# Performance work log

Hardware: AMD Instinct MI355X
Metric: run time of the kernel (lower is better)

Reference implementation:

```python
import jax, jax.numpy as jnp
import numpy as np

EPS = 1e-10


def spmm(rows, cols, vals, x, n_rows):
    # COO sparse [n_rows, *] @ dense x : out[r] = sum_e vals[e] * x[cols[e]]
    return jax.ops.segment_sum(vals[:, None] * x[cols], rows, num_segments=n_rows)


def setup_inputs() -> dict:
    key = jax.random.key(0)
    ks = jax.random.split(key, 16)
    n_in, n_full, n_nodes, d, nnz, n_out = 65536, 65536, 131072, 256, 262144, 16384
    return {
        "mu": jax.random.normal(ks[0], (n_in, d), jnp.float32),
        "var": jax.random.uniform(ks[1], (n_in, d), jnp.float32),
        "mu_history": jax.random.normal(ks[2], (n_nodes, d), jnp.float32),
        "var_history": jax.random.uniform(ks[3], (n_nodes, d), jnp.float32),
        "adj_vals": jax.random.uniform(ks[4], (nnz,), jnp.float32),
        "fadj_vals": jax.random.uniform(ks[5], (nnz,), jnp.float32),
        "madj_vals": jax.random.uniform(ks[6], (nnz,), jnp.float32),
        "adj_rows": jax.random.randint(ks[7], (nnz,), 0, n_out, jnp.int32),
        "adj_cols": jax.random.randint(ks[8], (nnz,), 0, n_in, jnp.int32),
        "fadj_rows": jax.random.randint(ks[9], (nnz,), 0, n_out, jnp.int32),
        "fadj_cols": jax.random.randint(ks[10], (nnz,), 0, n_full, jnp.int32),
        "madj_rows": jax.random.randint(ks[11], (nnz,), 0, n_out, jnp.int32),
        "madj_cols": jax.random.randint(ks[12], (nnz,), 0, n_in, jnp.int32),
        "ifield": jax.random.randint(ks[13], (n_in,), 0, n_nodes, jnp.int32),
        "ffield": jax.random.randint(ks[14], (n_full,), 0, n_nodes, jnp.int32),
        "n_out": n_out,
    }


def reference(mu, var, mu_history, var_history,
              adj_vals, fadj_vals, madj_vals,
              adj_rows, adj_cols, fadj_rows, fadj_cols, madj_rows, madj_cols,
              ifield, ffield, n_out):
    # VRAggregator._call, tuple-(mu, var) branch, normalization != 'gcn'
    mu_self = mu[:n_out]
    var_self = var[:n_out]
    delta_mu = mu - mu_history[ifield]          # [n_in, d]
    mu_bar = mu_history[ffield]                 # [n_full, d]
    sigma = jnp.sqrt(var)
    sigma_bar = jnp.sqrt(var_history[ifield])
    delta_sigma = sigma - sigma_bar
    var_bar = var_history[ffield]
    msigma = delta_sigma * sigma_bar
    mu_neighbour = (spmm(adj_rows, adj_cols, adj_vals, delta_mu, n_out)
                    + spmm(fadj_rows, fadj_cols, fadj_vals, mu_bar, n_out))
    var_neighbour = (spmm(adj_rows, adj_cols, adj_vals * adj_vals, delta_sigma * delta_sigma, n_out)
                     + spmm(fadj_rows, fadj_cols, fadj_vals * fadj_vals, var_bar, n_out)
                     + 2.0 * spmm(madj_rows, madj_cols, madj_vals, msigma, n_out))
    var_neighbour = jax.nn.relu(var_neighbour) + EPS
    return (jnp.concatenate((mu_self, mu_neighbour), axis=1),
            jnp.concatenate((var_self, var_neighbour), axis=1))
```

## Files before the change

### kernel.cpp

```cpp
#include <hip/hip_runtime.h>

#define EPS_F 1e-10f

typedef unsigned int u32;

__device__ __forceinline__ u32 bf16pair(float lo, float hi) {
  u32 a = __float_as_uint(lo);
  u32 b = __float_as_uint(hi);
  a = a + 0x7FFFu + ((a >> 16) & 1u);
  b = b + 0x7FFFu + ((b >> 16) & 1u);
  return (a >> 16) | (b & 0xFFFF0000u);
}
__device__ __forceinline__ float bf_lo(u32 u) { return __uint_as_float(u << 16); }
__device__ __forceinline__ float bf_hi(u32 u) { return __uint_as_float(u & 0xFFFF0000u); }

__device__ __forceinline__ void acc_am(float4& am, uint4 u, float W) {
  am.x += W * bf_lo(u.x); am.y += W * bf_hi(u.x);
  am.z += W * bf_lo(u.y); am.w += W * bf_hi(u.y);
}
__device__ __forceinline__ void acc_av(float4& av, uint4 u, float Q) {
  av.x += Q * bf_lo(u.z); av.y += Q * bf_hi(u.z);
  av.z += Q * bf_lo(u.w); av.w += Q * bf_hi(u.w);
}
__device__ __forceinline__ void acc_m(float4& av, uint2 x, float W) {
  av.x += W * bf_lo(x.x); av.y += W * bf_hi(x.x);
  av.z += W * bf_lo(x.y); av.w += W * bf_hi(x.y);
}

__global__ __launch_bounds__(256) void k_count(
    const int* __restrict__ ra, const int* __restrict__ rf,
    const int* __restrict__ rm, int* __restrict__ cnt, int nnz, int n_out) {
  int total = 3 * nnz;
  for (int i = blockIdx.x * blockDim.x + threadIdx.x; i < total;
       i += gridDim.x * blockDim.x) {
    int m = (i >= nnz) + (i >= 2 * nnz);
    int e = i - m * nnz;
    const int* rp = (m == 0) ? ra : (m == 1) ? rf : rm;
    atomicAdd(&cnt[m * n_out + rp[e]], 1);
  }
}

__global__ __launch_bounds__(256) void k_scan3(const int* __restrict__ cnt_all,
                                               int* __restrict__ base_all,
                                               int* __restrict__ cur_all, int n) {
  const int* cnt = cnt_all + blockIdx.x * n;
  int* base = base_all + blockIdx.x * (n + 1);
  int* cur = cur_all + blockIdx.x * n;
  __shared__ int sums[256];
  int tid = threadIdx.x;
  int chunk = (n + 255) / 256;
  int s = tid * chunk, e = min(s + chunk, n);
  int local = 0;
  for (int i = s; i < e; ++i) local += cnt[i];
  sums[tid] = local;
  __syncthreads();
  for (int off = 1; off < 256; off <<= 1) {
    int v = (tid >= off) ? sums[tid - off] : 0;
    __syncthreads();
    sums[tid] += v;
    __syncthreads();
  }
  int run = (tid == 0) ? 0 : sums[tid - 1];
  for (int i = s; i < e; ++i) {
    base[i] = run;
    cur[i] = run;
    run += cnt[i];
  }
  if (tid == 255) base[n] = sums[255];
}

template <bool WITH_FB>
__global__ __launch_bounds__(256) void k_pre_scatter(
    const float* __restrict__ mu, const float* __restrict__ var,
    const float* __restrict__ muh, const float* __restrict__ varh,
    const int* __restrict__ ifield, const int* __restrict__ ffield,
    const int* __restrict__ ra, const int* __restrict__ ca, const float* __restrict__ va,
    const int* __restrict__ rf, const int* __restrict__ cf, const float* __restrict__ vf,
    const int* __restrict__ rm, const int* __restrict__ cm, const float* __restrict__ vm,
    int* __restrict__ cur_all, uint2* __restrict__ ord,
    u32* __restrict__ A, u32* __restrict__ M, u32* __restrict__ FB,
    int n_in, int n_full, int n_out, int nnz) {
  int tid = blockIdx.x * blockDim.x + threadIdx.x;
  int nth = gridDim.x * blockDim.x;

  int total = 3 * nnz;
  for (int i = tid; i < total; i += nth) {
    int m = (i >= nnz) + (i >= 2 * nnz);
    int e = i - m * nnz;
    const int* rp = (m == 0) ? ra : (m == 1) ? rf : rm;
    const int* cp = (m == 0) ? ca : (m == 1) ? cf : cm;
    const float* vp = (m == 0) ? va : (m == 1) ? vf : vm;
    int r = rp[e];
    int c = cp[e];
    float w = vp[e];
    if (!WITH_FB && m == 1) c = ffield[c];
    if (m == 2) w = 2.0f * w;
    int pos = atomicAdd(&cur_all[m * n_out + r], 1);
    ord[(size_t)m * nnz + pos] = make_uint2((u32)c, __float_as_uint(w));
  }

  int wave = tid >> 6;
  int lane = tid & 63;
  int nw = nth >> 6;
  int nr = WITH_FB ? (n_in > n_full ? n_in : n_full) : n_in;
  int rpw = (nr + nw - 1) / nw;
  int r0 = wave * rpw;
  int r1 = min(nr, r0 + rpw);
  for (int row = r0; row < r1; ++row) {
    if (row < n_in) {
      int f = ifield[row];
      float4 m  = ((const float4*)(mu   + (size_t)row * 256))[lane];
      float4 v  = ((const float4*)(var  + (size_t)row * 256))[lane];
      float4 mh = ((const float4*)(muh  + (size_t)f   * 256))[lane];
      float4 vh = ((const float4*)(varh + (size_t)f   * 256))[lane];
      float4 d, q, p;
      float s, sb, ds;
      s = sqrtf(v.x); sb = sqrtf(vh.x); ds = s - sb; d.x = m.x - mh.x; q.x = ds * ds; p.x = ds * sb;
      s = sqrtf(v.y); sb = sqrtf(vh.y); ds = s - sb; d.y = m.y - mh.y; q.y = ds * ds; p.y = ds * sb;
      s = sqrtf(v.z); sb = sqrtf(vh.z); ds = s - sb; d.z = m.z - mh.z; q.z = ds * ds; p.z = ds * sb;
      s = sqrtf(v.w); sb = sqrtf(vh.w); ds = s - sb; d.w = m.w - mh.w; q.w = ds * ds; p.w = ds * sb;
      uint4 au;
      au.x = bf16pair(d.x, d.y);
      au.y = bf16pair(d.z, d.w);
      au.z = bf16pair(q.x, q.y);
      au.w = bf16pair(q.z, q.w);
      ((uint4*)(A + (size_t)row * 256))[lane] = au;
      uint2 mu2;
      mu2.x = bf16pair(p.x, p.y);
      mu2.y = bf16pair(p.z, p.w);
      ((uint2*)(M + (size_t)row * 128))[lane] = mu2;
    }
    if (WITH_FB && row < n_full) {
      int f = ffield[row];
      float4 mb = ((const float4*)(muh  + (size_t)f * 256))[lane];
      float4 vb = ((const float4*)(varh + (size_t)f * 256))[lane];
      uint4 fu;
      fu.x = bf16pair(mb.x, mb.y);
      fu.y = bf16pair(mb.z, mb.w);
      fu.z = bf16pair(vb.x, vb.y);
      fu.w = bf16pair(vb.z, vb.w);
      ((uint4*)(FB + (size_t)row * 256))[lane] = fu;
    }
  }
}

template <bool HAS_FB>
__global__ __launch_bounds__(256) void k_agg(
    const float* __restrict__ mu, const float* __restrict__ var,
    const float* __restrict__ muh, const float* __restrict__ varh,
    const u32* __restrict__ A, const u32* __restrict__ M,
    const u32* __restrict__ FB,
    const int* __restrict__ base_all, const uint2* __restrict__ ord,
    float* __restrict__ out0, float* __restrict__ out1, int n_out, int nnz) {
  int r = (int)((blockIdx.x * blockDim.x + threadIdx.x) >> 6);
  int lane = threadIdx.x & 63;
  if (r >= n_out) return;

  float4 msf = ((const float4*)(mu  + (size_t)r * 256))[lane];
  float4 vsf = ((const float4*)(var + (size_t)r * 256))[lane];

  float4 am = make_float4(0.f, 0.f, 0.f, 0.f);
  float4 av = make_float4(0.f, 0.f, 0.f, 0.f);

  {
    const int* base = base_all;
    const uint2* o = ord;
    int b0 = base[r], b1 = base[r + 1];
    int p = b0;
    for (; p + 3 < b1; p += 4) {
      uint2 cv0 = o[p], cv1 = o[p + 1], cv2 = o[p + 2], cv3 = o[p + 3];
      uint4 u0 = ((const uint4*)(A + (size_t)cv0.x * 256))[lane];
      uint4 u1 = ((const uint4*)(A + (size_t)cv1.x * 256))[lane];
      uint4 u2 = ((const uint4*)(A + (size_t)cv2.x * 256))[lane];
      uint4 u3 = ((const uint4*)(A + (size_t)cv3.x * 256))[lane];
      float w0 = __uint_as_float(cv0.y), w1 = __uint_as_float(cv1.y);
      float w2 = __uint_as_float(cv2.y), w3 = __uint_as_float(cv3.y);
      acc_am(am, u0, w0); acc_am(am, u1, w1); acc_am(am, u2, w2); acc_am(am, u3, w3);
      acc_av(av, u0, w0 * w0); acc_av(av, u1, w1 * w1);
      acc_av(av, u2, w2 * w2); acc_av(av, u3, w3 * w3);
    }
    for (; p < b1; ++p) {
      uint2 cv0 = o[p];
      float w0 = __uint_as_float(cv0.y);
      uint4 u0 = ((const uint4*)(A + (size_t)cv0.x * 256))[lane];
      acc_am(am, u0, w0); acc_av(av, u0, w0 * w0);
    }
  }

  {
    const int* base = base_all + (n_out + 1);
    const uint2* o = ord + (size_t)nnz;
    int b0 = base[r], b1 = base[r + 1];
    int p = b0;
    if (HAS_FB) {
      for (; p + 3 < b1; p += 4) {
        uint2 cv0 = o[p], cv1 = o[p + 1], cv2 = o[p + 2], cv3 = o[p + 3];
        uint4 u0 = ((const uint4*)(FB + (size_t)cv0.x * 256))[lane];
        uint4 u1 = ((const uint4*)(FB + (size_t)cv1.x * 256))[lane];
        uint4 u2 = ((const uint4*)(FB + (size_t)cv2.x * 256))[lane];
        uint4 u3 = ((const uint4*)(FB + (size_t)cv3.x * 256))[lane];
        float w0 = __uint_as_float(cv0.y), w1 = __uint_as_float(cv1.y);
        float w2 = __uint_as_float(cv2.y), w3 = __uint_as_float(cv3.y);
        acc_am(am, u0, w0); acc_am(am, u1, w1); acc_am(am, u2, w2); acc_am(am, u3, w3);
        acc_av(av, u0, w0 * w0); acc_av(av, u1, w1 * w1);
        acc_av(av, u2, w2 * w2); acc_av(av, u3, w3 * w3);
      }
      for (; p < b1; ++p) {
        uint2 cv0 = o[p];
        float w0 = __uint_as_float(cv0.y);
        uint4 u0 = ((const uint4*)(FB + (size_t)cv0.x * 256))[lane];
        acc_am(am, u0, w0); acc_av(av, u0, w0 * w0);
      }
    } else {
      for (; p + 1 < b1; p += 2) {
        uint2 cv0 = o[p], cv1 = o[p + 1];
        float w0 = __uint_as_float(cv0.y), w1 = __uint_as_float(cv1.y);
        float4 m0 = ((const float4*)(muh  + (size_t)cv0.x * 256))[lane];
        float4 v0 = ((const float4*)(varh + (size_t)cv0.x * 256))[lane];
        float4 m1 = ((const float4*)(muh  + (size_t)cv1.x * 256))[lane];
        float4 v1 = ((const float4*)(varh + (size_t)cv1.x * 256))[lane];
        float q0 = w0 * w0, q1 = w1 * w1;
        am.x += w0 * m0.x + w1 * m1.x; am.y += w0 * m0.y + w1 * m1.y;
        am.z += w0 * m0.z + w1 * m1.z; am.w += w0 * m0.w + w1 * m1.w;
        av.x += q0 * v0.x + q1 * v1.x; av.y += q0 * v0.y + q1 * v1.y;
        av.z += q0 * v0.z + q1 * v1.z; av.w += q0 * v0.w + q1 * v1.w;
      }
      if (p < b1) {
        uint2 cv0 = o[p];
        float w0 = __uint_as_float(cv0.y);
        float4 m0 = ((const float4*)(muh  + (size_t)cv0.x * 256))[lane];
        float4 v0 = ((const float4*)(varh + (size_t)cv0.x * 256))[lane];
        float q0 = w0 * w0;
        am.x += w0 * m0.x; am.y += w0 * m0.y; am.z += w0 * m0.z; am.w += w0 * m0.w;
        av.x += q0 * v0.x; av.y += q0 * v0.y; av.z += q0 * v0.z; av.w += q0 * v0.w;
      }
    }
  }

  {
    const int* base = base_all + 2 * (n_out + 1);
    const uint2* o = ord + 2 * (size_t)nnz;
    int b0 = base[r], b1 = base[r + 1];
    int p = b0;
    for (; p + 3 < b1; p += 4) {
      uint2 cv0 = o[p], cv1 = o[p + 1], cv2 = o[p + 2], cv3 = o[p + 3];
      uint2 x0 = ((const uint2*)(M + (size_t)cv0.x * 128))[lane];
      uint2 x1 = ((const uint2*)(M + (size_t)cv1.x * 128))[lane];
      uint2 x2 = ((const uint2*)(M + (size_t)cv2.x * 128))[lane];
      uint2 x3 = ((const uint2*)(M + (size_t)cv3.x * 128))[lane];
      float w0 = __uint_as_float(cv0.y), w1 = __uint_as_float(cv1.y);
      float w2 = __uint_as_float(cv2.y), w3 = __uint_as_float(cv3.y);
      acc_m(av, x0, w0); acc_m(av, x1, w1); acc_m(av, x2, w2); acc_m(av, x3, w3);
    }
    for (; p < b1; ++p) {
      uint2 cv0 = o[p];
      float w0 = __uint_as_float(cv0.y);
      uint2 x0 = ((const uint2*)(M + (size_t)cv0.x * 128))[lane];
      acc_m(av, x0, w0);
    }
  }

  av.x = fmaxf(av.x, 0.f) + EPS_F;
  av.y = fmaxf(av.y, 0.f) + EPS_F;
  av.z = fmaxf(av.z, 0.f) + EPS_F;
  av.w = fmaxf(av.w, 0.f) + EPS_F;
  ((float4*)(out0 + (size_t)r * 512))[lane]       = msf;
  ((float4*)(out0 + (size_t)r * 512 + 256))[lane] = am;
  ((float4*)(out1 + (size_t)r * 512))[lane]       = vsf;
  ((float4*)(out1 + (size_t)r * 512 + 256))[lane] = av;
}

__global__ __launch_bounds__(256) void k_init_out(
    const float* __restrict__ mu, const float* __restrict__ var,
    float* __restrict__ out0, float* __restrict__ out1) {
  int r = blockIdx.x;
  int t = threadIdx.x;
  const float4 z = make_float4(0.f, 0.f, 0.f, 0.f);
  if (t < 128) {
    float4* dst = (float4*)(out0 + (size_t)r * 512);
    dst[t] = (t < 64) ? ((const float4*)(mu + (size_t)r * 256))[t] : z;
  } else {
    int u = t - 128;
    float4* dst = (float4*)(out1 + (size_t)r * 512);
    dst[u] = (u < 64) ? ((const float4*)(var + (size_t)r * 256))[u] : z;
  }
}

__global__ __launch_bounds__(256) void k_edge_adj_fb(
    const float* __restrict__ vals, const int* __restrict__ rows,
    const int* __restrict__ cols,
    const float* __restrict__ mu, const float* __restrict__ var,
    const float* __restrict__ muh, const float* __restrict__ varh,
    const int* __restrict__ ifield,
    float* __restrict__ out0, float* __restrict__ out1, int nnz) {
  int wave = (int)((blockIdx.x * blockDim.x + threadIdx.x) >> 6);
  int lane = threadIdx.x & 63;
  int nw = (int)((gridDim.x * blockDim.x) >> 6);
  for (int e = wave; e < nnz; e += nw) {
    float w = vals[e];
    int r = rows[e];
    int c = cols[e];
    int f = ifield[c];
    float4 m  = ((const float4*)(mu   + (size_t)c * 256))[lane];
    float4 v  = ((const float4*)(var  + (size_t)c * 256))[lane];
    float4 mh = ((const float4*)(muh  + (size_t)f * 256))[lane];
    float4 vh = ((const float4*)(varh + (size_t)f * 256))[lane];
    float4 xm, xv;
    float ds;
    xm.x = m.x - mh.x; ds = sqrtf(v.x) - sqrtf(vh.x); xv.x = ds * ds;
    xm.y = m.y - mh.y; ds = sqrtf(v.y) - sqrtf(vh.y); xv.y = ds * ds;
    xm.z = m.z - mh.z; ds = sqrtf(v.z) - sqrtf(vh.z); xv.z = ds * ds;
    xm.w = m.w - mh.w; ds = sqrtf(v.w) - sqrtf(vh.w); xv.w = ds * ds;
    float w2 = w * w;
    float* om = out0 + (size_t)r * 512 + 256 + lane * 4;
    float* ov = out1 + (size_t)r * 512 + 256 + lane * 4;
    atomicAdd(om + 0, w * xm.x); atomicAdd(om + 1, w * xm.y);
    atomicAdd(om + 2, w * xm.z); atomicAdd(om + 3, w * xm.w);
    atomicAdd(ov + 0, w2 * xv.x); atomicAdd(ov + 1, w2 * xv.y);
    atomicAdd(ov + 2, w2 * xv.z); atomicAdd(ov + 3, w2 * xv.w);
  }
}

__global__ __launch_bounds__(256) void k_edge_fadj_fb(
    const float* __restrict__ vals, const int* __restrict__ rows,
    const int* __restrict__ cols,
    const float* __restrict__ muh, const float* __restrict__ varh,
    const int* __restrict__ ffield,
    float* __restrict__ out0, float* __restrict__ out1, int nnz) {
  int wave = (int)((blockIdx.x * blockDim.x + threadIdx.x) >> 6);
  int lane = threadIdx.x & 63;
  int nw = (int)((gridDim.x * blockDim.x) >> 6);
  for (int e = wave; e < nnz; e += nw) {
    float w = vals[e];
    int r = rows[e];
    int f = ffield[cols[e]];
    float4 mb = ((const float4*)(muh  + (size_t)f * 256))[lane];
    float4 vb = ((const float4*)(varh + (size_t)f * 256))[lane];
    float w2 = w * w;
    float* om = out0 + (size_t)r * 512 + 256 + lane * 4;
    float* ov = out1 + (size_t)r * 512 + 256 + lane * 4;
    atomicAdd(om + 0, w * mb.x); atomicAdd(om + 1, w * mb.y);
    atomicAdd(om + 2, w * mb.z); atomicAdd(om + 3, w * mb.w);
    atomicAdd(ov + 0, w2 * vb.x); atomicAdd(ov + 1, w2 * vb.y);
    atomicAdd(ov + 2, w2 * vb.z); atomicAdd(ov + 3, w2 * vb.w);
  }
}

__global__ __launch_bounds__(256) void k_edge_madj_fb(
    const float* __restrict__ vals, const int* __restrict__ rows,
    const int* __restrict__ cols,
    const float* __restrict__ var, const float* __restrict__ varh,
    const int* __restrict__ ifield,
    float* __restrict__ out1, int nnz) {
  int wave = (int)((blockIdx.x * blockDim.x + threadIdx.x) >> 6);
  int lane = threadIdx.x & 63;
  int nw = (int)((gridDim.x * blockDim.x) >> 6);
  for (int e = wave; e < nnz; e += nw) {
    float w = 2.0f * vals[e];
    int r = rows[e];
    int c = cols[e];
    int f = ifield[c];
    float4 v  = ((const float4*)(var  + (size_t)c * 256))[lane];
    float4 vh = ((const float4*)(varh + (size_t)f * 256))[lane];
    float4 x;
    float sb;
    sb = sqrtf(vh.x); x.x = (sqrtf(v.x) - sb) * sb;
    sb = sqrtf(vh.y); x.y = (sqrtf(v.y) - sb) * sb;
    sb = sqrtf(vh.z); x.z = (sqrtf(v.z) - sb) * sb;
    sb = sqrtf(vh.w); x.w = (sqrtf(v.w) - sb) * sb;
    float* ov = out1 + (size_t)r * 512 + 256 + lane * 4;
    atomicAdd(ov + 0, w * x.x); atomicAdd(ov + 1, w * x.y);
    atomicAdd(ov + 2, w * x.z); atomicAdd(ov + 3, w * x.w);
  }
}

__global__ __launch_bounds__(256) void k_final(float* __restrict__ out1, int n_out) {
  int total = n_out * 64;
  for (int i = blockIdx.x * blockDim.x + threadIdx.x; i < total;
       i += gridDim.x * blockDim.x) {
    int r = i >> 6;
    int q = i & 63;
    float4* p = (float4*)(out1 + (size_t)r * 512 + 256) + q;
    float4 v = *p;
    v.x = fmaxf(v.x, 0.f) + EPS_F;
    v.y = fmaxf(v.y, 0.f) + EPS_F;
    v.z = fmaxf(v.z, 0.f) + EPS_F;
    v.w = fmaxf(v.w, 0.f) + EPS_F;
    *p = v;
  }
}

extern "C" void kernel_launch(void* const* d_in, const int* in_sizes, int n_in_args,
                              void* d_out, int out_size, void* d_ws, size_t ws_size,
                              hipStream_t stream) {
  const float* mu        = (const float*)d_in[0];
  const float* var       = (const float*)d_in[1];
  const float* muh       = (const float*)d_in[2];
  const float* varh      = (const float*)d_in[3];
  const float* adj_vals  = (const float*)d_in[4];
  const float* fadj_vals = (const float*)d_in[5];
  const float* madj_vals = (const float*)d_in[6];
  const int* adj_rows    = (const int*)d_in[7];
  const int* adj_cols    = (const int*)d_in[8];
  const int* fadj_rows   = (const int*)d_in[9];
  const int* fadj_cols   = (const int*)d_in[10];
  const int* madj_rows   = (const int*)d_in[11];
  const int* madj_cols   = (const int*)d_in[12];
  const int* ifield      = (const int*)d_in[13];
  const int* ffield      = (const int*)d_in[14];

  const int n_out  = out_size / 1024;
  const int n_in   = in_sizes[0] / 256;
  const int nnz    = in_sizes[4];
  const int n_full = in_sizes[14];

  float* out0 = (float*)d_out;
  float* out1 = out0 + (size_t)n_out * 512;

  const size_t uA = (size_t)n_in * 256;
  const size_t uM = (size_t)n_in * 128;
  const size_t uFB = (size_t)n_full * 256;
  const size_t uOrd = (size_t)3 * nnz * 2;
  const size_t uCnt = (size_t)3 * n_out;
  const size_t uBase = (size_t)3 * (n_out + 1);
  const size_t need2 = (uA + uM + uOrd + uCnt + uBase + uCnt) * sizeof(u32);
  const size_t need1 = need2 + uFB * sizeof(u32);

  if (ws_size >= need2) {
    const bool fb = (ws_size >= need1);
    u32* A = (u32*)d_ws;
    u32* M = A + uA;
    u32* FB = M + uM;
    u32* tail = fb ? (FB + uFB) : (M + uM);
    uint2* ord = (uint2*)tail;
    int* cnt  = (int*)(tail + uOrd);
    int* base = cnt + uCnt;
    int* cur  = base + uBase;

    (void)hipMemsetAsync(cnt, 0, uCnt * sizeof(int), stream);
    k_count<<<1024, 256, 0, stream>>>(adj_rows, fadj_rows, madj_rows, cnt, nnz, n_out);
    k_scan3<<<3, 256, 0, stream>>>(cnt, base, cur, n_out);
    if (fb) {
      k_pre_scatter<true><<<2048, 256, 0, stream>>>(
          mu, var, muh, varh, ifield, ffield,
          adj_rows, adj_cols, adj_vals, fadj_rows, fadj_cols, fadj_vals,
          madj_rows, madj_cols, madj_vals,
          cur, ord, A, M, FB, n_in, n_full, n_out, nnz);
    } else {
      k_pre_scatter<false><<<2048, 256, 0, stream>>>(
          mu, var, muh, varh, ifield, ffield,
          adj_rows, adj_cols, adj_vals, fadj_rows, fadj_cols, fadj_vals,
          madj_rows, madj_cols, madj_vals,
          cur, ord, A, M, nullptr, n_in, n_full, n_out, nnz);
    }
    int blocks = (n_out * 64 + 255) / 256;
    if (fb) {
      k_agg<true><<<blocks, 256, 0, stream>>>(mu, var, muh, varh, A, M, FB, base, ord,
                                              out0, out1, n_out, nnz);
    } else {
      k_agg<false><<<blocks, 256, 0, stream>>>(mu, var, muh, varh, A, M, nullptr, base, ord,
                                               out0, out1, n_out, nnz);
    }
  } else {
    k_init_out<<<n_out, 256, 0, stream>>>(mu, var, out0, out1);
    k_edge_adj_fb<<<4096, 256, 0, stream>>>(adj_vals, adj_rows, adj_cols,
                                            mu, var, muh, varh, ifield, out0, out1, nnz);
    k_edge_madj_fb<<<4096, 256, 0, stream>>>(madj_vals, madj_rows, madj_cols,
                                             var, varh, ifield, out1, nnz);
    k_edge_fadj_fb<<<4096, 256, 0, stream>>>(fadj_vals, fadj_rows, fadj_cols,
                                             muh, varh, ffield, out0, out1, nnz);
    k_final<<<4096, 256, 0, stream>>>(out1, n_out);
  }
}
```

Measured before the change: 310.7 us.

## Pack full history table to bf16 once and gather through it

Instead of building a per-full-row bf16 FB table (gathering history rows via ffield), the count kernel now converts the entire mu/var history table (n_nodes rows) to packed bf16 in a contiguous streaming pass. The pre-scatter kernel resolves fadj columns through ffield into node indices, and reads the history for delta computation from the bf16 table. This removes a random gather of fp32 history in pre-scatter, but the table now has n_nodes rows instead of n_full, so more bytes are written. Reading history in bf16 before the subtraction and sqrt also adds precision error to delta_mu and sigma_bar.

```diff
diff --git a/kernel.cpp b/kernel.cpp
--- a/kernel.cpp
+++ b/kernel.cpp
@@ -27,16 +27,38 @@
   av.z += W * bf_lo(x.y); av.w += W * bf_hi(x.y);
 }
 
-__global__ __launch_bounds__(256) void k_count(
+template <bool WITH_HB>
+__global__ __launch_bounds__(256) void k_hist_count(
+    const float* __restrict__ muh, const float* __restrict__ varh,
+    u32* __restrict__ HB, int n_nodes,
     const int* __restrict__ ra, const int* __restrict__ rf,
     const int* __restrict__ rm, int* __restrict__ cnt, int nnz, int n_out) {
+  int tid = blockIdx.x * blockDim.x + threadIdx.x;
+  int nth = gridDim.x * blockDim.x;
+
   int total = 3 * nnz;
-  for (int i = blockIdx.x * blockDim.x + threadIdx.x; i < total;
-       i += gridDim.x * blockDim.x) {
+  for (int i = tid; i < total; i += nth) {
     int m = (i >= nnz) + (i >= 2 * nnz);
     int e = i - m * nnz;
     const int* rp = (m == 0) ? ra : (m == 1) ? rf : rm;
     atomicAdd(&cnt[m * n_out + rp[e]], 1);
+  }
+
+  if (WITH_HB) {
+    int wave = tid >> 6, lane = tid & 63, nw = nth >> 6;
+    int rpw = (n_nodes + nw - 1) / nw;
+    int r0 = wave * rpw;
+    int r1 = min(n_nodes, r0 + rpw);
+    for (int node = r0; node < r1; ++node) {
+      float4 mh = ((const float4*)(muh  + (size_t)node * 256))[lane];
+      float4 vh = ((const float4*)(varh + (size_t)node * 256))[lane];
+      uint4 hu;
+      hu.x = bf16pair(mh.x, mh.y);
+      hu.y = bf16pair(mh.z, mh.w);
+      hu.z = bf16pair(vh.x, vh.y);
+      hu.w = bf16pair(vh.z, vh.w);
+      ((uint4*)(HB + (size_t)node * 256))[lane] = hu;
+    }
   }
 }
 
@@ -69,17 +91,18 @@
   if (tid == 255) base[n] = sums[255];
 }
 
-template <bool WITH_FB>
+template <bool WITH_HB>
 __global__ __launch_bounds__(256) void k_pre_scatter(
     const float* __restrict__ mu, const float* __restrict__ var,
     const float* __restrict__ muh, const float* __restrict__ varh,
+    const u32* __restrict__ HB,
     const int* __restrict__ ifield, const int* __restrict__ ffield,
     const int* __restrict__ ra, const int* __restrict__ ca, const float* __restrict__ va,
     const int* __restrict__ rf, const int* __restrict__ cf, const float* __restrict__ vf,
     const int* __restrict__ rm, const int* __restrict__ cm, const float* __restrict__ vm,
     int* __restrict__ cur_all, uint2* __restrict__ ord,
-    u32* __restrict__ A, u32* __restrict__ M, u32* __restrict__ FB,
-    int n_in, int n_full, int n_out, int nnz) {
+    u32* __restrict__ A, u32* __restrict__ M,
+    int n_in, int n_out, int nnz) {
   int tid = blockIdx.x * blockDim.x + threadIdx.x;
   int nth = gridDim.x * blockDim.x;
 
@@ -93,63 +116,54 @@
     int r = rp[e];
     int c = cp[e];
     float w = vp[e];
-    if (!WITH_FB && m == 1) c = ffield[c];
+    if (m == 1) c = ffield[c];
     if (m == 2) w = 2.0f * w;
     int pos = atomicAdd(&cur_all[m * n_out + r], 1);
     ord[(size_t)m * nnz + pos] = make_uint2((u32)c, __float_as_uint(w));
   }
 
-  int wave = tid >> 6;
-  int lane = tid & 63;
-  int nw = nth >> 6;
-  int nr = WITH_FB ? (n_in > n_full ? n_in : n_full) : n_in;
-  int rpw = (nr + nw - 1) / nw;
+  int wave = tid >> 6, lane = tid & 63, nw = nth >> 6;
+  int rpw = (n_in + nw - 1) / nw;
   int r0 = wave * rpw;
-  int r1 = min(nr, r0 + rpw);
+  int r1 = min(n_in, r0 + rpw);
   for (int row = r0; row < r1; ++row) {
-    if (row < n_in) {
-      int f = ifield[row];
-      float4 m  = ((const float4*)(mu   + (size_t)row * 256))[lane];
-      float4 v  = ((const float4*)(var  + (size_t)row * 256))[lane];
-      float4 mh = ((const float4*)(muh  + (size_t)f   * 256))[lane];
-      float4 vh = ((const float4*)(varh + (size_t)f   * 256))[lane];
-      float4 d, q, p;
-      float s, sb, ds;
-      s = sqrtf(v.x); sb = sqrtf(vh.x); ds = s - sb; d.x = m.x - mh.x; q.x = ds * ds; p.x = ds * sb;
-      s = sqrtf(v.y); sb = sqrtf(vh.y); ds = s - sb; d.y = m.y - mh.y; q.y = ds * ds; p.y = ds * sb;
-      s = sqrtf(v.z); sb = sqrtf(vh.z); ds = s - sb; d.z = m.z - mh.z; q.z = ds * ds; p.z = ds * sb;
-      s = sqrtf(v.w); sb = sqrtf(vh.w); ds = s - sb; d.w = m.w - mh.w; q.w = ds * ds; p.w = ds * sb;
-      uint4 au;
-      au.x = bf16pair(d.x, d.y);
-      au.y = bf16pair(d.z, d.w);
-      au.z = bf16pair(q.x, q.y);
-      au.w = bf16pair(q.z, q.w);
-      ((uint4*)(A + (size_t)row * 256))[lane] = au;
-      uint2 mu2;
-      mu2.x = bf16pair(p.x, p.y);
-      mu2.y = bf16pair(p.z, p.w);
-      ((uint2*)(M + (size_t)row * 128))[lane] = mu2;
-    }
-    if (WITH_FB && row < n_full) {
-      int f = ffield[row];
-      float4 mb = ((const float4*)(muh  + (size_t)f * 256))[lane];
-      float4 vb = ((const float4*)(varh + (size_t)f * 256))[lane];
-      uint4 fu;
-      fu.x = bf16pair(mb.x, mb.y);
-      fu.y = bf16pair(mb.z, mb.w);
-      fu.z = bf16pair(vb.x, vb.y);
-      fu.w = bf16pair(vb.z, vb.w);
-      ((uint4*)(FB + (size_t)row * 256))[lane] = fu;
-    }
-  }
-}
-
-template <bool HAS_FB>
+    int f = ifield[row];
+    float4 m  = ((const float4*)(mu  + (size_t)row * 256))[lane];
+    float4 v  = ((const float4*)(var + (size_t)row * 256))[lane];
+    float4 mh, vh;
+    if (WITH_HB) {
+      uint4 h = ((const uint4*)(HB + (size_t)f * 256))[lane];
+      mh = make_float4(bf_lo(h.x), bf_hi(h.x), bf_lo(h.y), bf_hi(h.y));
+      vh = make_float4(bf_lo(h.z), bf_hi(h.z), bf_lo(h.w), bf_hi(h.w));
+    } else {
+      mh = ((const float4*)(muh  + (size_t)f * 256))[lane];
+      vh = ((const float4*)(varh + (size_t)f * 256))[lane];
+    }
+    float4 d, q, p;
+    float s, sb, ds;
+    s = sqrtf(v.x); sb = sqrtf(vh.x); ds = s - sb; d.x = m.x - mh.x; q.x = ds * ds; p.x = ds * sb;
+    s = sqrtf(v.y); sb = sqrtf(vh.y); ds = s - sb; d.y = m.y - mh.y; q.y = ds * ds; p.y = ds * sb;
+    s = sqrtf(v.z); sb = sqrtf(vh.z); ds = s - sb; d.z = m.z - mh.z; q.z = ds * ds; p.z = ds * sb;
+    s = sqrtf(v.w); sb = sqrtf(vh.w); ds = s - sb; d.w = m.w - mh.w; q.w = ds * ds; p.w = ds * sb;
+    uint4 au;
+    au.x = bf16pair(d.x, d.y);
+    au.y = bf16pair(d.z, d.w);
+    au.z = bf16pair(q.x, q.y);
+    au.w = bf16pair(q.z, q.w);
+    ((uint4*)(A + (size_t)row * 256))[lane] = au;
+    uint2 mu2;
+    mu2.x = bf16pair(p.x, p.y);
+    mu2.y = bf16pair(p.z, p.w);
+    ((uint2*)(M + (size_t)row * 128))[lane] = mu2;
+  }
+}
+
+template <bool HAS_HB>
 __global__ __launch_bounds__(256) void k_agg(
     const float* __restrict__ mu, const float* __restrict__ var,
     const float* __restrict__ muh, const float* __restrict__ varh,
     const u32* __restrict__ A, const u32* __restrict__ M,
-    const u32* __restrict__ FB,
+    const u32* __restrict__ HB,
     const int* __restrict__ base_all, const uint2* __restrict__ ord,
     float* __restrict__ out0, float* __restrict__ out1, int n_out, int nnz) {
   int r = (int)((blockIdx.x * blockDim.x + threadIdx.x) >> 6);
@@ -192,13 +206,13 @@
     const uint2* o = ord + (size_t)nnz;
     int b0 = base[r], b1 = base[r + 1];
     int p = b0;
-    if (HAS_FB) {
+    if (HAS_HB) {
       for (; p + 3 < b1; p += 4) {
         uint2 cv0 = o[p], cv1 = o[p + 1], cv2 = o[p + 2], cv3 = o[p + 3];
-        uint4 u0 = ((const uint4*)(FB + (size_t)cv0.x * 256))[lane];
-        uint4 u1 = ((const uint4*)(FB + (size_t)cv1.x * 256))[lane];
-        uint4 u2 = ((const uint4*)(FB + (size_t)cv2.x * 256))[lane];
-        uint4 u3 = ((const uint4*)(FB + (size_t)cv3.x * 256))[lane];
+        uint4 u0 = ((const uint4*)(HB + (size_t)cv0.x * 256))[lane];
+        uint4 u1 = ((const uint4*)(HB + (size_t)cv1.x * 256))[lane];
+        uint4 u2 = ((const uint4*)(HB + (size_t)cv2.x * 256))[lane];
+        uint4 u3 = ((const uint4*)(HB + (size_t)cv3.x * 256))[lane];
         float w0 = __uint_as_float(cv0.y), w1 = __uint_as_float(cv1.y);
         float w2 = __uint_as_float(cv2.y), w3 = __uint_as_float(cv3.y);
         acc_am(am, u0, w0); acc_am(am, u1, w1); acc_am(am, u2, w2); acc_am(am, u3, w3);
@@ -208,7 +222,7 @@
       for (; p < b1; ++p) {
         uint2 cv0 = o[p];
         float w0 = __uint_as_float(cv0.y);
-        uint4 u0 = ((const uint4*)(FB + (size_t)cv0.x * 256))[lane];
+        uint4 u0 = ((const uint4*)(HB + (size_t)cv0.x * 256))[lane];
         acc_am(am, u0, w0); acc_av(av, u0, w0 * w0);
       }
     } else {
@@ -409,53 +423,61 @@
   const int* ifield      = (const int*)d_in[13];
   const int* ffield      = (const int*)d_in[14];
 
-  const int n_out  = out_size / 1024;
-  const int n_in   = in_sizes[0] / 256;
-  const int nnz    = in_sizes[4];
-  const int n_full = in_sizes[14];
+  const int n_out   = out_size / 1024;
+  const int n_in    = in_sizes[0] / 256;
+  const int nnz     = in_sizes[4];
+  const int n_nodes = in_sizes[2] / 256;
 
   float* out0 = (float*)d_out;
   float* out1 = out0 + (size_t)n_out * 512;
 
   const size_t uA = (size_t)n_in * 256;
   const size_t uM = (size_t)n_in * 128;
-  const size_t uFB = (size_t)n_full * 256;
+  const size_t uHB = (size_t)n_nodes * 256;
   const size_t uOrd = (size_t)3 * nnz * 2;
   const size_t uCnt = (size_t)3 * n_out;
   const size_t uBase = (size_t)3 * (n_out + 1);
   const size_t need2 = (uA + uM + uOrd + uCnt + uBase + uCnt) * sizeof(u32);
-  const size_t need1 = need2 + uFB * sizeof(u32);
+  const size_t need1 = need2 + uHB * sizeof(u32);
 
   if (ws_size >= need2) {
-    const bool fb = (ws_size >= need1);
+    const bool hb = (ws_size >= need1);
     u32* A = (u32*)d_ws;
     u32* M = A + uA;
-    u32* FB = M + uM;
-    u32* tail = fb ? (FB + uFB) : (M + uM);
+    u32* HB = M + uM;
+    u32* tail = hb ? (HB + uHB) : (M + uM);
     uint2* ord = (uint2*)tail;
     int* cnt  = (int*)(tail + uOrd);
     int* base = cnt + uCnt;
     int* cur  = base + uBase;
 
     (void)hipMemsetAsync(cnt, 0, uCnt * sizeof(int), stream);
-    k_count<<<1024, 256, 0, stream>>>(adj_rows, fadj_rows, madj_rows, cnt, nnz, n_out);
+    if (hb) {
+      k_hist_count<true><<<4096, 256, 0, stream>>>(muh, varh, HB, n_nodes,
+                                                   adj_rows, fadj_rows, madj_rows,
+                                                   cnt, nnz, n_out);
+    } else {
+      k_hist_count<false><<<1024, 256, 0, stream>>>(muh, varh, nullptr, n_nodes,
+                                                    adj_rows, fadj_rows, madj_rows,
+                                                    cnt, nnz, n_out);
+    }
     k_scan3<<<3, 256, 0, stream>>>(cnt, base, cur, n_out);
-    if (fb) {
+    if (hb) {
       k_pre_scatter<true><<<2048, 256, 0, stream>>>(
-          mu, var, muh, varh, ifield, ffield,
+          mu, var, muh, varh, HB, ifield, ffield,
           adj_rows, adj_cols, adj_vals, fadj_rows, fadj_cols, fadj_vals,
           madj_rows, madj_cols, madj_vals,
-          cur, ord, A, M, FB, n_in, n_full, n_out, nnz);
+          cur, ord, A, M, n_in, n_out, nnz);
     } else {
       k_pre_scatter<false><<<2048, 256, 0, stream>>>(
-          mu, var, muh, varh, ifield, ffield,
+          mu, var, muh, varh, nullptr, ifield, ffield,
           adj_rows, adj_cols, adj_vals, fadj_rows, fadj_cols, fadj_vals,
           madj_rows, madj_cols, madj_vals,
-          cur, ord, A, M, nullptr, n_in, n_full, n_out, nnz);
+          cur, ord, A, M, n_in, n_out, nnz);
     }
     int blocks = (n_out * 64 + 255) / 256;
-    if (fb) {
-      k_agg<true><<<blocks, 256, 0, stream>>>(mu, var, muh, varh, A, M, FB, base, ord,
+    if (hb) {
+      k_agg<true><<<blocks, 256, 0, stream>>>(mu, var, muh, varh, A, M, HB, base, ord,
                                               out0, out1, n_out, nnz);
     } else {
       k_agg<false><<<blocks, 256, 0, stream>>>(mu, var, muh, varh, A, M, nullptr, base, ord,
```

New measurement: 340.4 us. +9.6%, slower.

## Batch edge-list loads with wave shuffles and move self-copy into pre-scatter

Applied to the files above, without the earlier changes.

In the aggregation kernel, each wave now loads up to 64 (col, weight) pairs with one coalesced load and broadcasts them with __shfl. Before, every lane loaded each pair redundantly inside the gather loop. The copy of mu/var into the first half of the outputs moves from the aggregation kernel into the preprocessing kernel, which already reads those rows, so the separate reload is gone. The preprocessing row loop is split into separate n_in and n_full passes. This trades extra shuffle instructions for fewer scalar/vector index loads, and it shifts some output writes earlier in the schedule.

```diff
diff --git a/kernel.cpp b/kernel.cpp
--- a/kernel.cpp
+++ b/kernel.cpp
@@ -79,6 +79,7 @@
     const int* __restrict__ rm, const int* __restrict__ cm, const float* __restrict__ vm,
     int* __restrict__ cur_all, uint2* __restrict__ ord,
     u32* __restrict__ A, u32* __restrict__ M, u32* __restrict__ FB,
+    float* __restrict__ out0, float* __restrict__ out1,
     int n_in, int n_full, int n_out, int nnz) {
   int tid = blockIdx.x * blockDim.x + threadIdx.x;
   int nth = gridDim.x * blockDim.x;
@@ -99,15 +100,13 @@
     ord[(size_t)m * nnz + pos] = make_uint2((u32)c, __float_as_uint(w));
   }
 
-  int wave = tid >> 6;
-  int lane = tid & 63;
-  int nw = nth >> 6;
-  int nr = WITH_FB ? (n_in > n_full ? n_in : n_full) : n_in;
-  int rpw = (nr + nw - 1) / nw;
-  int r0 = wave * rpw;
-  int r1 = min(nr, r0 + rpw);
-  for (int row = r0; row < r1; ++row) {
-    if (row < n_in) {
+  int wave = tid >> 6, lane = tid & 63, nw = nth >> 6;
+
+  {
+    int rpw = (n_in + nw - 1) / nw;
+    int r0 = wave * rpw;
+    int r1 = min(n_in, r0 + rpw);
+    for (int row = r0; row < r1; ++row) {
       int f = ifield[row];
       float4 m  = ((const float4*)(mu   + (size_t)row * 256))[lane];
       float4 v  = ((const float4*)(var  + (size_t)row * 256))[lane];
@@ -129,8 +128,18 @@
       mu2.x = bf16pair(p.x, p.y);
       mu2.y = bf16pair(p.z, p.w);
       ((uint2*)(M + (size_t)row * 128))[lane] = mu2;
-    }
-    if (WITH_FB && row < n_full) {
+      if (row < n_out) {
+        ((float4*)(out0 + (size_t)row * 512))[lane] = m;
+        ((float4*)(out1 + (size_t)row * 512))[lane] = v;
+      }
+    }
+  }
+
+  if (WITH_FB) {
+    int rpw = (n_full + nw - 1) / nw;
+    int r0 = wave * rpw;
+    int r1 = min(n_full, r0 + rpw);
+    for (int row = r0; row < r1; ++row) {
       int f = ffield[row];
       float4 mb = ((const float4*)(muh  + (size_t)f * 256))[lane];
       float4 vb = ((const float4*)(varh + (size_t)f * 256))[lane];
@@ -146,7 +155,6 @@
 
 template <bool HAS_FB>
 __global__ __launch_bounds__(256) void k_agg(
-    const float* __restrict__ mu, const float* __restrict__ var,
     const float* __restrict__ muh, const float* __restrict__ varh,
     const u32* __restrict__ A, const u32* __restrict__ M,
     const u32* __restrict__ FB,
@@ -156,34 +164,37 @@
   int lane = threadIdx.x & 63;
   if (r >= n_out) return;
 
-  float4 msf = ((const float4*)(mu  + (size_t)r * 256))[lane];
-  float4 vsf = ((const float4*)(var + (size_t)r * 256))[lane];
-
   float4 am = make_float4(0.f, 0.f, 0.f, 0.f);
   float4 av = make_float4(0.f, 0.f, 0.f, 0.f);
 
   {
-    const int* base = base_all;
+    int b0 = base_all[r], b1 = base_all[r + 1];
     const uint2* o = ord;
-    int b0 = base[r], b1 = base[r + 1];
-    int p = b0;
-    for (; p + 3 < b1; p += 4) {
-      uint2 cv0 = o[p], cv1 = o[p + 1], cv2 = o[p + 2], cv3 = o[p + 3];
-      uint4 u0 = ((const uint4*)(A + (size_t)cv0.x * 256))[lane];
-      uint4 u1 = ((const uint4*)(A + (size_t)cv1.x * 256))[lane];
-      uint4 u2 = ((const uint4*)(A + (size_t)cv2.x * 256))[lane];
-      uint4 u3 = ((const uint4*)(A + (size_t)cv3.x * 256))[lane];
-      float w0 = __uint_as_float(cv0.y), w1 = __uint_as_float(cv1.y);
-      float w2 = __uint_as_float(cv2.y), w3 = __uint_as_float(cv3.y);
-      acc_am(am, u0, w0); acc_am(am, u1, w1); acc_am(am, u2, w2); acc_am(am, u3, w3);
-      acc_av(av, u0, w0 * w0); acc_av(av, u1, w1 * w1);
-      acc_av(av, u2, w2 * w2); acc_av(av, u3, w3 * w3);
-    }
-    for (; p < b1; ++p) {
-      uint2 cv0 = o[p];
-      float w0 = __uint_as_float(cv0.y);
-      uint4 u0 = ((const uint4*)(A + (size_t)cv0.x * 256))[lane];
-      acc_am(am, u0, w0); acc_av(av, u0, w0 * w0);
+    for (int s = b0; s < b1; s += 64) {
+      int rem = min(64, b1 - s);
+      uint2 cv = (lane < rem) ? o[s + lane] : make_uint2(0u, 0u);
+      int j = 0;
+      for (; j + 3 < rem; j += 4) {
+        int c0 = __shfl((int)cv.x, j),     c1 = __shfl((int)cv.x, j + 1);
+        int c2 = __shfl((int)cv.x, j + 2), c3 = __shfl((int)cv.x, j + 3);
+        float w0 = __uint_as_float((u32)__shfl((int)cv.y, j));
+        float w1 = __uint_as_float((u32)__shfl((int)cv.y, j + 1));
+        float w2 = __uint_as_float((u32)__shfl((int)cv.y, j + 2));
+        float w3 = __uint_as_float((u32)__shfl((int)cv.y, j + 3));
+        uint4 u0 = ((const uint4*)(A + (size_t)(u32)c0 * 256))[lane];
+        uint4 u1 = ((const uint4*)(A + (size_t)(u32)c1 * 256))[lane];
+        uint4 u2 = ((const uint4*)(A + (size_t)(u32)c2 * 256))[lane];
+        uint4 u3 = ((const uint4*)(A + (size_t)(u32)c3 * 256))[lane];
+        acc_am(am, u0, w0); acc_am(am, u1, w1); acc_am(am, u2, w2); acc_am(am, u3, w3);
+        acc_av(av, u0, w0 * w0); acc_av(av, u1, w1 * w1);
+        acc_av(av, u2, w2 * w2); acc_av(av, u3, w3 * w3);
+      }
+      for (; j < rem; ++j) {
+        int c0 = __shfl((int)cv.x, j);
+        float w0 = __uint_as_float((u32)__shfl((int)cv.y, j));
+        uint4 u0 = ((const uint4*)(A + (size_t)(u32)c0 * 256))[lane];
+        acc_am(am, u0, w0); acc_av(av, u0, w0 * w0);
+      }
     }
   }
 
@@ -191,48 +202,42 @@
     const int* base = base_all + (n_out + 1);
     const uint2* o = ord + (size_t)nnz;
     int b0 = base[r], b1 = base[r + 1];
-    int p = b0;
-    if (HAS_FB) {
-      for (; p + 3 < b1; p += 4) {
-        uint2 cv0 = o[p], cv1 = o[p + 1], cv2 = o[p + 2], cv3 = o[p + 3];
-        uint4 u0 = ((const uint4*)(FB + (size_t)cv0.x * 256))[lane];
-        uint4 u1 = ((const uint4*)(FB + (size_t)cv1.x * 256))[lane];
-        uint4 u2 = ((const uint4*)(FB + (size_t)cv2.x * 256))[lane];
-        uint4 u3 = ((const uint4*)(FB + (size_t)cv3.x * 256))[lane];
-        float w0 = __uint_as_float(cv0.y), w1 = __uint_as_float(cv1.y);
-        float w2 = __uint_as_float(cv2.y), w3 = __uint_as_float(cv3.y);
-        acc_am(am, u0, w0); acc_am(am, u1, w1); acc_am(am, u2, w2); acc_am(am, u3, w3);
-        acc_av(av, u0, w0 * w0); acc_av(av, u1, w1 * w1);
-        acc_av(av, u2, w2 * w2); acc_av(av, u3, w3 * w3);
-      }
-      for (; p < b1; ++p) {
-        uint2 cv0 = o[p];
-        float w0 = __uint_as_float(cv0.y);
-        uint4 u0 = ((const uint4*)(FB + (size_t)cv0.x * 256))[lane];
-        acc_am(am, u0, w0); acc_av(av, u0, w0 * w0);
-      }
-    } else {
-      for (; p + 1 < b1; p += 2) {
-        uint2 cv0 = o[p], cv1 = o[p + 1];
-        float w0 = __uint_as_float(cv0.y), w1 = __uint_as_float(cv1.y);
-        float4 m0 = ((const float4*)(muh  + (size_t)cv0.x * 256))[lane];
-        float4 v0 = ((const float4*)(varh + (size_t)cv0.x * 256))[lane];
-        float4 m1 = ((const float4*)(muh  + (size_t)cv1.x * 256))[lane];
-        float4 v1 = ((const float4*)(varh + (size_t)cv1.x * 256))[lane];
-        float q0 = w0 * w0, q1 = w1 * w1;
-        am.x += w0 * m0.x + w1 * m1.x; am.y += w0 * m0.y + w1 * m1.y;
-        am.z += w0 * m0.z + w1 * m1.z; am.w += w0 * m0.w + w1 * m1.w;
-        av.x += q0 * v0.x + q1 * v1.x; av.y += q0 * v0.y + q1 * v1.y;
-        av.z += q0 * v0.z + q1 * v1.z; av.w += q0 * v0.w + q1 * v1.w;
-      }
-      if (p < b1) {
-        uint2 cv0 = o[p];
-        float w0 = __uint_as_float(cv0.y);
-        float4 m0 = ((const float4*)(muh  + (size_t)cv0.x * 256))[lane];
-        float4 v0 = ((const float4*)(varh + (size_t)cv0.x * 256))[lane];
-        float q0 = w0 * w0;
-        am.x += w0 * m0.x; am.y += w0 * m0.y; am.z += w0 * m0.z; am.w += w0 * m0.w;
-        av.x += q0 * v0.x; av.y += q0 * v0.y; av.z += q0 * v0.z; av.w += q0 * v0.w;
+    for (int s = b0; s < b1; s += 64) {
+      int rem = min(64, b1 - s);
+      uint2 cv = (lane < rem) ? o[s + lane] : make_uint2(0u, 0u);
+      int j = 0;
+      if (HAS_FB) {
+        for (; j + 3 < rem; j += 4) {
+          int c0 = __shfl((int)cv.x, j),     c1 = __shfl((int)cv.x, j + 1);
+          int c2 = __shfl((int)cv.x, j + 2), c3 = __shfl((int)cv.x, j + 3);
+          float w0 = __uint_as_float((u32)__shfl((int)cv.y, j));
+          float w1 = __uint_as_float((u32)__shfl((int)cv.y, j + 1));
+          float w2 = __uint_as_float((u32)__shfl((int)cv.y, j + 2));
+          float w3 = __uint_as_float((u32)__shfl((int)cv.y, j + 3));
+          uint4 u0 = ((const uint4*)(FB + (size_t)(u32)c0 * 256))[lane];
+          uint4 u1 = ((const uint4*)(FB + (size_t)(u32)c1 * 256))[lane];
+          uint4 u2 = ((const uint4*)(FB + (size_t)(u32)c2 * 256))[lane];
+          uint4 u3 = ((const uint4*)(FB + (size_t)(u32)c3 * 256))[lane];
+          acc_am(am, u0, w0); acc_am(am, u1, w1); acc_am(am, u2, w2); acc_am(am, u3, w3);
+          acc_av(av, u0, w0 * w0); acc_av(av, u1, w1 * w1);
+          acc_av(av, u2, w2 * w2); acc_av(av, u3, w3 * w3);
+        }
+        for (; j < rem; ++j) {
+          int c0 = __shfl((int)cv.x, j);
+          float w0 = __uint_as_float((u32)__shfl((int)cv.y, j));
+          uint4 u0 = ((const uint4*)(FB + (size_t)(u32)c0 * 256))[lane];
+          acc_am(am, u0, w0); acc_av(av, u0, w0 * w0);
+        }
+      } else {
+        for (; j < rem; ++j) {
+          int c0 = __shfl((int)cv.x, j);
+          float w0 = __uint_as_float((u32)__shfl((int)cv.y, j));
+          float4 m0 = ((const float4*)(muh  + (size_t)(u32)c0 * 256))[lane];
+          float4 v0 = ((const float4*)(varh + (size_t)(u32)c0 * 256))[lane];
+          float q0 = w0 * w0;
+          am.x += w0 * m0.x; am.y += w0 * m0.y; am.z += w0 * m0.z; am.w += w0 * m0.w;
+          av.x += q0 * v0.x; av.y += q0 * v0.y; av.z += q0 * v0.z; av.w += q0 * v0.w;
+        }
       }
     }
   }
@@ -241,22 +246,29 @@
     const int* base = base_all + 2 * (n_out + 1);
     const uint2* o = ord + 2 * (size_t)nnz;
     int b0 = base[r], b1 = base[r + 1];
-    int p = b0;
-    for (; p + 3 < b1; p += 4) {
-      uint2 cv0 = o[p], cv1 = o[p + 1], cv2 = o[p + 2], cv3 = o[p + 3];
-      uint2 x0 = ((const uint2*)(M + (size_t)cv0.x * 128))[lane];
-      uint2 x1 = ((const uint2*)(M + (size_t)cv1.x * 128))[lane];
-      uint2 x2 = ((const uint2*)(M + (size_t)cv2.x * 128))[lane];
-      uint2 x3 = ((const uint2*)(M + (size_t)cv3.x * 128))[lane];
-      float w0 = __uint_as_float(cv0.y), w1 = __uint_as_float(cv1.y);
-      float w2 = __uint_as_float(cv2.y), w3 = __uint_as_float(cv3.y);
-      acc_m(av, x0, w0); acc_m(av, x1, w1); acc_m(av, x2, w2); acc_m(av, x3, w3);
-    }
-    for (; p < b1; ++p) {
-      uint2 cv0 = o[p];
-      float w0 = __uint_as_float(cv0.y);
-      uint2 x0 = ((const uint2*)(M + (size_t)cv0.x * 128))[lane];
-      acc_m(av, x0, w0);
+    for (int s = b0; s < b1; s += 64) {
+      int rem = min(64, b1 - s);
+      uint2 cv = (lane < rem) ? o[s + lane] : make_uint2(0u, 0u);
+      int j = 0;
+      for (; j + 3 < rem; j += 4) {
+        int c0 = __shfl((int)cv.x, j),     c1 = __shfl((int)cv.x, j + 1);
+        int c2 = __shfl((int)cv.x, j + 2), c3 = __shfl((int)cv.x, j + 3);
+        float w0 = __uint_as_float((u32)__shfl((int)cv.y, j));
+        float w1 = __uint_as_float((u32)__shfl((int)cv.y, j + 1));
+        float w2 = __uint_as_float((u32)__shfl((int)cv.y, j + 2));
+        float w3 = __uint_as_float((u32)__shfl((int)cv.y, j + 3));
+        uint2 x0 = ((const uint2*)(M + (size_t)(u32)c0 * 128))[lane];
+        uint2 x1 = ((const uint2*)(M + (size_t)(u32)c1 * 128))[lane];
+        uint2 x2 = ((const uint2*)(M + (size_t)(u32)c2 * 128))[lane];
+        uint2 x3 = ((const uint2*)(M + (size_t)(u32)c3 * 128))[lane];
+        acc_m(av, x0, w0); acc_m(av, x1, w1); acc_m(av, x2, w2); acc_m(av, x3, w3);
+      }
+      for (; j < rem; ++j) {
+        int c0 = __shfl((int)cv.x, j);
+        float w0 = __uint_as_float((u32)__shfl((int)cv.y, j));
+        uint2 x0 = ((const uint2*)(M + (size_t)(u32)c0 * 128))[lane];
+        acc_m(av, x0, w0);
+      }
     }
   }
 
@@ -264,9 +276,7 @@
   av.y = fmaxf(av.y, 0.f) + EPS_F;
   av.z = fmaxf(av.z, 0.f) + EPS_F;
   av.w = fmaxf(av.w, 0.f) + EPS_F;
-  ((float4*)(out0 + (size_t)r * 512))[lane]       = msf;
   ((float4*)(out0 + (size_t)r * 512 + 256))[lane] = am;
-  ((float4*)(out1 + (size_t)r * 512))[lane]       = vsf;
   ((float4*)(out1 + (size_t)r * 512 + 256))[lane] = av;
 }
 
@@ -445,20 +455,20 @@
           mu, var, muh, varh, ifield, ffield,
           adj_rows, adj_cols, adj_vals, fadj_rows, fadj_cols, fadj_vals,
           madj_rows, madj_cols, madj_vals,
-          cur, ord, A, M, FB, n_in, n_full, n_out, nnz);
+          cur, ord, A, M, FB, out0, out1, n_in, n_full, n_out, nnz);
     } else {
       k_pre_scatter<false><<<2048, 256, 0, stream>>>(
           mu, var, muh, varh, ifield, ffield,
           adj_rows, adj_cols, adj_vals, fadj_rows, fadj_cols, fadj_vals,
           madj_rows, madj_cols, madj_vals,
-          cur, ord, A, M, nullptr, n_in, n_full, n_out, nnz);
+          cur, ord, A, M, nullptr, out0, out1, n_in, n_full, n_out, nnz);
     }
     int blocks = (n_out * 64 + 255) / 256;
     if (fb) {
-      k_agg<true><<<blocks, 256, 0, stream>>>(mu, var, muh, varh, A, M, FB, base, ord,
+      k_agg<true><<<blocks, 256, 0, stream>>>(muh, varh, A, M, FB, base, ord,
                                               out0, out1, n_out, nnz);
     } else {
-      k_agg<false><<<blocks, 256, 0, stream>>>(mu, var, muh, varh, A, M, nullptr, base, ord,
+      k_agg<false><<<blocks, 256, 0, stream>>>(muh, varh, A, M, nullptr, base, ord,
                                                out0, out1, n_out, nnz);
     }
   } else {
```

Result: faster. 304.1 us (-2.1%).
